# Kernel tuning notes

Measured on AMD Instinct MI355X. Metric: run time of the kernel, lower is better.

Reference implementation:

```python
import jax, jax.numpy as jnp
import numpy as np

B, S, D = 32, 256, 512   # batch, seq, shared_base hdim
N, H, O = 16, 256, 2     # num_tasks heads, adapter hidden, output_dim
VOCAB = 1024             # property-token lookup table length


def setup_inputs() -> dict:
    key = jax.random.key(0)
    ks = jax.random.split(key, 10)
    adapter_input = jax.random.normal(ks[0], (B, S, D), dtype=jnp.float32)
    tasks = jax.random.randint(ks[1], (B, S), 0, VOCAB, dtype=jnp.int64)
    lookup_table = jax.random.randint(ks[2], (VOCAB,), 0, N, dtype=jnp.int64)
    s1 = 1.0 / np.sqrt(D)
    s2 = 1.0 / np.sqrt(H)
    W1 = jax.random.uniform(ks[3], (N, D, H), jnp.float32, -s1, s1)
    b1 = jax.random.uniform(ks[4], (N, H), jnp.float32, -s1, s1)
    W2 = jax.random.uniform(ks[5], (N, H, H), jnp.float32, -s2, s2)
    b2 = jax.random.uniform(ks[6], (N, H), jnp.float32, -s2, s2)
    W3 = jax.random.uniform(ks[7], (N, H, O), jnp.float32, -s2, s2)
    b3 = jax.random.uniform(ks[8], (N, O), jnp.float32, -s2, s2)
    return dict(adapter_input=adapter_input, tasks=tasks, lookup_table=lookup_table,
                W1=W1, b1=b1, W2=W2, b2=b2, W3=W3, b3=b3)


def reference(adapter_input, tasks, lookup_table, W1, b1, W2, b2, W3, b3):
    # --- PropertyToIndexRouter: task token -> head index (-1 if out of range / unmapped)
    L = lookup_table.shape[0]
    clamped = jnp.clip(tasks, 0, L - 1)
    head_indices = lookup_table[clamped]
    invalid = (tasks >= L) | (tasks < 0)
    head_indices = jnp.where(invalid, -1, head_indices)          # [B, S]

    valid = head_indices >= 0
    idx = jnp.where(valid, head_indices, 0)                      # safe gather index

    # --- each head's SimpleAdapter run densely over all tokens (dropout=eval no-op),
    # vectorized over the head dim instead of a Python loop per head
    h1 = jax.nn.relu(jnp.einsum('bsd,ndh->bsnh', adapter_input, W1) + b1)   # [B,S,N,H]
    h2 = jax.nn.relu(jnp.einsum('bsnh,nhk->bsnk', h1, W2) + b2)             # [B,S,N,H]
    out_all = jnp.einsum('bsnk,nko->bsno', h2, W3) + b3                     # [B,S,N,O]

    # --- masked scatter-combine: pick each token's assigned head, zeros elsewhere
    out = jnp.take_along_axis(out_all, idx[:, :, None, None], axis=2)[:, :, 0, :]  # [B,S,O]
    out = jnp.where(valid[:, :, None], out, jnp.zeros((), out.dtype))
    return out
```

## Files before the change

### kernel.cpp

```cpp
#include <hip/hip_runtime.h>

#define TOK_TOTAL 8192
#define DDIM 512
#define HDIM 256
#define ODIM 2
#define NHEADS 16
#define VOCAB 1024

typedef __attribute__((ext_vector_type(8))) short short8;
typedef __attribute__((ext_vector_type(4))) float f32x4;
typedef __attribute__((ext_vector_type(4))) unsigned short ushort4v;

__device__ inline ushort f2bf(float f) {
    uint u = __float_as_uint(f);
    uint r = (u + 0x7fffu + ((u >> 16) & 1u)) >> 16;
    return (ushort)r;
}
__device__ inline float bf2f(ushort h) { return __uint_as_float(((uint)h) << 16); }

__global__ __launch_bounds__(256) void mth_prep_route(
    const float* __restrict__ W1, const float* __restrict__ W2,
    const int* __restrict__ tasks, const int* __restrict__ lut,
    ushort* __restrict__ W1h, ushort* __restrict__ W2h,
    int* __restrict__ counts, int* __restrict__ lists,
    float* __restrict__ out)
{
    const int b = blockIdx.x, t = threadIdx.x;

    if (b < 384) {
        __shared__ float s[32][257];
        const float* src;
        ushort* dh;
        if (b < 256) {
            const int n = b >> 4, kc = b & 15;
            src = W1 + (size_t)(n * 16 + kc) * 8192;
            dh  = W1h + (size_t)(n * 16 + kc) * 8192;
        } else {
            const int b2 = b - 256, n = b2 >> 3, kc = b2 & 7;
            src = W2 + (size_t)(n * 8 + kc) * 8192;
            dh  = W2h + (size_t)(n * 8 + kc) * 8192;
        }
        #pragma unroll
        for (int i = 0; i < 8; ++i) {
            const int q = t + i * 256;
            const float4 f = ((const float4*)src)[q];
            const int k = q >> 6, c4 = (q & 63) * 4;
            s[k][c4] = f.x; s[k][c4 + 1] = f.y; s[k][c4 + 2] = f.z; s[k][c4 + 3] = f.w;
        }
        __syncthreads();
        #pragma unroll
        for (int i = 0; i < 4; ++i) {
            const int s8 = t + i * 256;
            const int lidx = s8 & 63;
            const int c = (s8 >> 6) * 16 + (lidx & 15);
            const int kw = (lidx >> 4) * 8;
            short8 hb;
            #pragma unroll
            for (int j = 0; j < 8; ++j) hb[j] = (short)f2bf(s[kw + j][c]);
            *(short8*)(dh + (size_t)s8 * 8) = hb;
        }
        return;
    }

    const int i = b - 384;
    __shared__ int hist[16];
    __shared__ int wcnt[4][16];
    if (t < 16) hist[t] = 0;
    __syncthreads();
    for (int q = t; q < i * 256; q += 256) {
        const int task = tasks[q];
        const int h = (task >= 0 && task < VOCAB) ? lut[task] : -1;
        if (h >= 0) atomicAdd(&hist[h], 1);
    }
    const int tok = i * 256 + t;
    const int task = tasks[tok];
    const int h = (task >= 0 && task < VOCAB) ? lut[task] : -1;
    if (h < 0) {
        out[(size_t)tok * 2]     = 0.f;
        out[(size_t)tok * 2 + 1] = 0.f;
    }
    const int w = t >> 6, l = t & 63;
    const unsigned long long lt = (1ULL << l) - 1ULL;
    int pre = 0;
    #pragma unroll
    for (int n = 0; n < NHEADS; ++n) {
        const unsigned long long m = __ballot(h == n);
        if (h == n) pre = (int)__popcll(m & lt);
        if (l == 0) wcnt[w][n] = (int)__popcll(m);
    }
    __syncthreads();
    if (h >= 0) {
        int off = hist[h];
        for (int w2 = 0; w2 < w; ++w2) off += wcnt[w2][h];
        lists[h * TOK_TOTAL + off + pre] = tok;
    }
    if (i == 31 && t < 16) {
        int tot = hist[t];
        #pragma unroll
        for (int w2 = 0; w2 < 4; ++w2) tot += wcnt[w2][t];
        counts[t] = tot;
    }
}

__global__ __launch_bounds__(256) void mth_mlp4(
    const float* __restrict__ X, const int* __restrict__ counts,
    const int* __restrict__ lists,
    const ushort* __restrict__ W1h, const ushort* __restrict__ W2h,
    const float* __restrict__ b1, const float* __restrict__ b2,
    const float* __restrict__ W3, const float* __restrict__ b3,
    float* __restrict__ out)
{
    __shared__ __align__(16) ushort Ah[16][64][8];
    __shared__ __align__(16) ushort Al[16][64][8];
    __shared__ __align__(16) ushort Hh[8][64][8];
    __shared__ __align__(16) ushort Hl[8][64][8];
    __shared__ float part[4][16][2];

    const int b = blockIdx.x;
    const int n = ((b & 7) << 1) | ((b >> 3) & 1);
    const int tile0 = b >> 4;

    const int tid = threadIdx.x;
    const int w   = tid >> 6;
    const int l   = tid & 63;
    const int r16 = l & 15;
    const int kg  = l >> 4;

    const int cnt = counts[n];
    const int listbase = n * TOK_TOTAL;

    float bias1[4], bias2[4];
    float2 w3v[4];
    #pragma unroll
    for (int cf = 0; cf < 4; ++cf) {
        const int col = w * 64 + cf * 16 + r16;
        bias1[cf] = b1[n * HDIM + col];
        bias2[cf] = b2[n * HDIM + col];
        w3v[cf]   = *(const float2*)(W3 + (size_t)(n * HDIM + col) * 2);
    }
    const ushort* w1hn = W1h + (size_t)n * (16 * 8192);
    const ushort* w2hn = W2h + (size_t)n * (8 * 8192);
    const int le8 = l * 8;

    for (int T = tile0; T * 16 < cnt; T += 64) {
        #pragma unroll
        for (int p = 0; p < 8; ++p) {
            const int q   = tid + p * 256;
            const int row = q >> 7;
            const int f4  = q & 127;
            const int tokidx = min(T * 16 + row, cnt - 1);
            const int tok = lists[listbase + tokidx];
            const float4 f = *(const float4*)(X + (size_t)tok * DDIM + f4 * 4);
            const int kc  = f4 >> 3;
            const int kgw = (f4 >> 1) & 3;
            const int j0  = (f4 & 1) * 4;
            const int ln2 = (kgw * 16 + row) ^ (kc & 7);
            ushort4v hv, lv;
            const float vv[4] = {f.x, f.y, f.z, f.w};
            #pragma unroll
            for (int e = 0; e < 4; ++e) {
                const uint u = __float_as_uint(vv[e]);
                hv[e] = (ushort)(u >> 16);
                lv[e] = f2bf(vv[e] - __uint_as_float(u & 0xffff0000u));
            }
            *(ushort4v*)&Ah[kc][ln2][j0] = hv;
            *(ushort4v*)&Al[kc][ln2][j0] = lv;
        }
        __syncthreads();

        f32x4 acc[4];
        #pragma unroll
        for (int cf = 0; cf < 4; ++cf) acc[cf] = (f32x4){0.f, 0.f, 0.f, 0.f};

        #pragma unroll 4
        for (int kc = 0; kc < 16; ++kc) {
            const int ls = l ^ (kc & 7);
            const short8 ah = *(const short8*)&Ah[kc][ls][0];
            const short8 al = *(const short8*)&Al[kc][ls][0];
            const ushort* bp = w1hn + kc * 8192 + le8;
            #pragma unroll
            for (int cf = 0; cf < 4; ++cf) {
                const short8 bh = *(const short8*)(bp + (w * 4 + cf) * 512);
                acc[cf] = __builtin_amdgcn_mfma_f32_16x16x32_bf16(ah, bh, acc[cf], 0, 0, 0);
                acc[cf] = __builtin_amdgcn_mfma_f32_16x16x32_bf16(al, bh, acc[cf], 0, 0, 0);
            }
        }

        #pragma unroll
        for (int cf = 0; cf < 4; ++cf) {
            const int kc2 = 2 * w + (cf >> 1);
            const int lp  = ((cf & 1) * 2 + (r16 >> 3)) * 16;
            const int e   = r16 & 7;
            #pragma unroll
            for (int j = 0; j < 4; ++j) {
                const float v = fmaxf(acc[cf][j] + bias1[cf], 0.f);
                const uint u = __float_as_uint(v);
                Hh[kc2][lp + kg * 4 + j][e] = (ushort)(u >> 16);
                Hl[kc2][lp + kg * 4 + j][e] =
                    f2bf(v - __uint_as_float(u & 0xffff0000u));
            }
        }
        __syncthreads();

        f32x4 acc2[4];
        #pragma unroll
        for (int cf = 0; cf < 4; ++cf) acc2[cf] = (f32x4){0.f, 0.f, 0.f, 0.f};

        #pragma unroll 4
        for (int kc = 0; kc < 8; ++kc) {
            const short8 ah = *(const short8*)&Hh[kc][l][0];
            const short8 al = *(const short8*)&Hl[kc][l][0];
            const ushort* bp = w2hn + kc * 8192 + le8;
            #pragma unroll
            for (int cf = 0; cf < 4; ++cf) {
                const short8 bh = *(const short8*)(bp + (w * 4 + cf) * 512);
                acc2[cf] = __builtin_amdgcn_mfma_f32_16x16x32_bf16(ah, bh, acc2[cf], 0, 0, 0);
                acc2[cf] = __builtin_amdgcn_mfma_f32_16x16x32_bf16(al, bh, acc2[cf], 0, 0, 0);
            }
        }

        float p[4][2];
        #pragma unroll
        for (int j = 0; j < 4; ++j) { p[j][0] = 0.f; p[j][1] = 0.f; }
        #pragma unroll
        for (int cf = 0; cf < 4; ++cf) {
            #pragma unroll
            for (int j = 0; j < 4; ++j) {
                const float v = fmaxf(acc2[cf][j] + bias2[cf], 0.f);
                p[j][0] = fmaf(v, w3v[cf].x, p[j][0]);
                p[j][1] = fmaf(v, w3v[cf].y, p[j][1]);
            }
        }
        #pragma unroll
        for (int off = 8; off >= 1; off >>= 1) {
            #pragma unroll
            for (int j = 0; j < 4; ++j) {
                p[j][0] += __shfl_xor(p[j][0], off);
                p[j][1] += __shfl_xor(p[j][1], off);
            }
        }
        if (r16 == 0) {
            #pragma unroll
            for (int j = 0; j < 4; ++j) {
                part[w][kg * 4 + j][0] = p[j][0];
                part[w][kg * 4 + j][1] = p[j][1];
            }
        }
        __syncthreads();

        if (tid < 32) {
            const int tk = tid >> 1, o = tid & 1;
            if (T * 16 + tk < cnt) {
                const float s = part[0][tk][o] + part[1][tk][o] +
                                part[2][tk][o] + part[3][tk][o];
                const int tok = lists[listbase + T * 16 + tk];
                out[(size_t)tok * 2 + o] = s + b3[n * 2 + o];
            }
        }
        __syncthreads();
    }
}

#define CHUNKS 16
#define CHUNK (TOK_TOTAL / CHUNKS)
#define TILE 32
#define KB 16

__global__ __launch_bounds__(256) void mth_routed_fp32(
    const float* __restrict__ X, const int* __restrict__ tasks,
    const int* __restrict__ lut,
    const float* __restrict__ W1, const float* __restrict__ b1,
    const float* __restrict__ W2, const float* __restrict__ b2,
    const float* __restrict__ W3, const float* __restrict__ b3,
    float* __restrict__ out)
{
    const int n = blockIdx.x, chnk = blockIdx.y, tid = threadIdx.x;
    const int lane = tid & 63, wv = tid >> 6, tx = tid & 31, ty = tid >> 5;
    __shared__ int s_list[CHUNK];
    __shared__ int s_cnt[8];
    __shared__ __align__(16) float s_x[KB][TILE];
    __shared__ __align__(16) float s_w[KB][HDIM];
    __shared__ __align__(16) float s_h[HDIM][TILE];
    const int base = chnk * CHUNK;
    int mytok[2], mypre[2], myseg[2]; bool mymatch[2];
    #pragma unroll
    for (int i = 0; i < 2; ++i) {
        const int tok = base + i * 256 + tid;
        const int task = tasks[tok];
        const int hidx = (task >= 0 && task < VOCAB) ? lut[task] : -1;
        const bool match = (hidx == n);
        const unsigned long long mask = __ballot(match);
        mytok[i] = tok; mymatch[i] = match;
        mypre[i] = __popcll(mask & ((1ULL << lane) - 1ULL));
        myseg[i] = i * 4 + wv;
        if (lane == 0) s_cnt[i * 4 + wv] = (int)__popcll(mask);
    }
    __syncthreads();
    int total = 0; int myoff[2] = {0, 0};
    #pragma unroll
    for (int s2 = 0; s2 < 8; ++s2) {
        if (s2 == myseg[0]) myoff[0] = total;
        if (s2 == myseg[1]) myoff[1] = total;
        total += s_cnt[s2];
    }
    #pragma unroll
    for (int i = 0; i < 2; ++i)
        if (mymatch[i]) s_list[myoff[i] + mypre[i]] = mytok[i];
    __syncthreads();
    const int ntok = total;
    if (ntok == 0) return;
    float bias1[8], bias2[8];
    #pragma unroll
    for (int j = 0; j < 8; ++j) {
        bias1[j] = b1[n * HDIM + tx * 8 + j];
        bias2[j] = b2[n * HDIM + tx * 8 + j];
    }
    float w3v[16];
    #pragma unroll
    for (int j = 0; j < 16; ++j) w3v[j] = W3[n * HDIM * ODIM + tx * 8 * ODIM + j];
    const float b3v0 = b3[n * ODIM + 0], b3v1 = b3[n * ODIM + 1];
    const float* W1n = W1 + (size_t)n * DDIM * HDIM;
    const float* W2n = W2 + (size_t)n * HDIM * HDIM;
    for (int ts = 0; ts < ntok; ts += TILE) {
        const int m = min(TILE, ntok - ts);
        float acc[4][8];
        #pragma unroll
        for (int t = 0; t < 4; ++t)
            #pragma unroll
            for (int j = 0; j < 8; ++j) acc[t][j] = 0.f;
        for (int kc = 0; kc < DDIM / KB; ++kc) {
            const float4* src = (const float4*)(W1n + kc * KB * HDIM);
            float4* dst = (float4*)s_w;
            #pragma unroll
            for (int p = 0; p < 4; ++p) dst[tid + p * 256] = src[tid + p * 256];
            #pragma unroll
            for (int p = 0; p < 2; ++p) {
                const int e = tid + p * 256;
                const int dd = e >> 5, t = e & 31;
                float v = 0.f;
                if (t < m) v = X[(size_t)s_list[ts + t] * DDIM + kc * KB + dd];
                s_x[dd][t] = v;
            }
            __syncthreads();
            #pragma unroll
            for (int dd = 0; dd < KB; ++dd) {
                const float4 xa = *(const float4*)&s_x[dd][ty * 4];
                const float4 wa = *(const float4*)&s_w[dd][tx * 8];
                const float4 wb = *(const float4*)&s_w[dd][tx * 8 + 4];
                const float xs[4] = {xa.x, xa.y, xa.z, xa.w};
                const float ws[8] = {wa.x, wa.y, wa.z, wa.w, wb.x, wb.y, wb.z, wb.w};
                #pragma unroll
                for (int t = 0; t < 4; ++t)
                    #pragma unroll
                    for (int j = 0; j < 8; ++j) acc[t][j] = fmaf(xs[t], ws[j], acc[t][j]);
            }
            __syncthreads();
        }
        #pragma unroll
        for (int j = 0; j < 8; ++j) {
            float4 v;
            v.x = fmaxf(acc[0][j] + bias1[j], 0.f);
            v.y = fmaxf(acc[1][j] + bias1[j], 0.f);
            v.z = fmaxf(acc[2][j] + bias1[j], 0.f);
            v.w = fmaxf(acc[3][j] + bias1[j], 0.f);
            *(float4*)&s_h[tx * 8 + j][ty * 4] = v;
        }
        __syncthreads();
        float acc2[4][8];
        #pragma unroll
        for (int t = 0; t < 4; ++t)
            #pragma unroll
            for (int j = 0; j < 8; ++j) acc2[t][j] = 0.f;
        for (int kc = 0; kc < HDIM / KB; ++kc) {
            const float4* src = (const float4*)(W2n + kc * KB * HDIM);
            float4* dst = (float4*)s_w;
            #pragma unroll
            for (int p = 0; p < 4; ++p) dst[tid + p * 256] = src[tid + p * 256];
            __syncthreads();
            #pragma unroll
            for (int dd = 0; dd < KB; ++dd) {
                const int k = kc * KB + dd;
                const float4 xa = *(const float4*)&s_h[k][ty * 4];
                const float4 wa = *(const float4*)&s_w[dd][tx * 8];
                const float4 wb = *(const float4*)&s_w[dd][tx * 8 + 4];
                const float xs[4] = {xa.x, xa.y, xa.z, xa.w};
                const float ws[8] = {wa.x, wa.y, wa.z, wa.w, wb.x, wb.y, wb.z, wb.w};
                #pragma unroll
                for (int t = 0; t < 4; ++t)
                    #pragma unroll
                    for (int j = 0; j < 8; ++j) acc2[t][j] = fmaf(xs[t], ws[j], acc2[t][j]);
            }
            __syncthreads();
        }
        float p0[4] = {0.f, 0.f, 0.f, 0.f}, p1[4] = {0.f, 0.f, 0.f, 0.f};
        #pragma unroll
        for (int t = 0; t < 4; ++t)
            #pragma unroll
            for (int j = 0; j < 8; ++j) {
                const float v = fmaxf(acc2[t][j] + bias2[j], 0.f);
                p0[t] = fmaf(v, w3v[j * 2 + 0], p0[t]);
                p1[t] = fmaf(v, w3v[j * 2 + 1], p1[t]);
            }
        #pragma unroll
        for (int off = 16; off > 0; off >>= 1)
            #pragma unroll
            for (int t = 0; t < 4; ++t) {
                p0[t] += __shfl_xor(p0[t], off);
                p1[t] += __shfl_xor(p1[t], off);
            }
        if (tx == 0) {
            #pragma unroll
            for (int t = 0; t < 4; ++t) {
                const int ti = ty * 4 + t;
                if (ti < m) {
                    const int tok = s_list[ts + ti];
                    out[tok * ODIM + 0] = p0[t] + b3v0;
                    out[tok * ODIM + 1] = p1[t] + b3v1;
                }
            }
        }
        __syncthreads();
    }
}

extern "C" void kernel_launch(void* const* d_in, const int* in_sizes, int n_in,
                              void* d_out, int out_size, void* d_ws, size_t ws_size,
                              hipStream_t stream) {
    (void)in_sizes; (void)n_in;
    const float* X     = (const float*)d_in[0];
    const int*   tasks = (const int*)d_in[1];
    const int*   lut   = (const int*)d_in[2];
    const float* W1    = (const float*)d_in[3];
    const float* b1    = (const float*)d_in[4];
    const float* W2    = (const float*)d_in[5];
    const float* b2    = (const float*)d_in[6];
    const float* W3    = (const float*)d_in[7];
    const float* b3    = (const float*)d_in[8];
    float* out = (float*)d_out;

    const size_t OFF_COUNTS = 0;
    const size_t OFF_LISTS  = 64;
    const size_t OFF_W1H    = OFF_LISTS + (size_t)NHEADS * TOK_TOTAL * 4;
    const size_t NW1        = (size_t)NHEADS * DDIM * HDIM;
    const size_t NW2        = (size_t)NHEADS * HDIM * HDIM;
    const size_t OFF_W2H    = OFF_W1H + NW1 * 2;
    const size_t NEED       = OFF_W2H + NW2 * 2;

    if (ws_size < NEED) {
        hipMemsetAsync(out, 0, (size_t)out_size * sizeof(float), stream);
        dim3 grid(NHEADS, CHUNKS);
        mth_routed_fp32<<<grid, 256, 0, stream>>>(X, tasks, lut, W1, b1, W2, b2, W3, b3, out);
        return;
    }

    char* ws = (char*)d_ws;
    int*    counts = (int*)(ws + OFF_COUNTS);
    int*    lists  = (int*)(ws + OFF_LISTS);
    ushort* W1h    = (ushort*)(ws + OFF_W1H);
    ushort* W2h    = (ushort*)(ws + OFF_W2H);

    mth_prep_route<<<416, 256, 0, stream>>>(W1, W2, tasks, lut,
                                            W1h, W2h, counts, lists, out);
    mth_mlp4<<<1024, 256, 0, stream>>>(X, counts, lists, W1h, W2h,
                                       b1, b2, W3, b3, out);
}
```

Before: 33.98 us.

## Process 32-token tiles per block with 8 waves sharing weight loads

The MLP kernel now uses 512-thread blocks that handle two 16-token sub-tiles at once. Waves are split into a token half and a column group, so each block's W1/W2 fragment loads serve twice as many tokens. The grid shrinks from 1024 to 256 blocks. This roughly halves per-token global weight traffic and the per-tile sync and epilogue overhead, but gives fewer blocks, doubles LDS per block, and wastes more padding work for heads with small token counts.

After: 41.94 us. +23.4%, slower.

```diff
diff --git a/kernel.cpp b/kernel.cpp
--- a/kernel.cpp
+++ b/kernel.cpp
@@ -102,7 +102,7 @@
     }
 }
 
-__global__ __launch_bounds__(256) void mth_mlp4(
+__global__ __launch_bounds__(512) void mth_mlp5(
     const float* __restrict__ X, const int* __restrict__ counts,
     const int* __restrict__ lists,
     const ushort* __restrict__ W1h, const ushort* __restrict__ W2h,
@@ -110,11 +110,11 @@
     const float* __restrict__ W3, const float* __restrict__ b3,
     float* __restrict__ out)
 {
-    __shared__ __align__(16) ushort Ah[16][64][8];
-    __shared__ __align__(16) ushort Al[16][64][8];
-    __shared__ __align__(16) ushort Hh[8][64][8];
-    __shared__ __align__(16) ushort Hl[8][64][8];
-    __shared__ float part[4][16][2];
+    __shared__ __align__(16) ushort Ah[16][2][64][8];
+    __shared__ __align__(16) ushort Al[16][2][64][8];
+    __shared__ __align__(16) ushort Hh[8][2][64][8];
+    __shared__ __align__(16) ushort Hl[8][2][64][8];
+    __shared__ float part[8][16][2];
 
     const int b = blockIdx.x;
     const int n = ((b & 7) << 1) | ((b >> 3) & 1);
@@ -122,6 +122,8 @@
 
     const int tid = threadIdx.x;
     const int w   = tid >> 6;
+    const int tf  = w >> 2;
+    const int cg  = w & 3;
     const int l   = tid & 63;
     const int r16 = l & 15;
     const int kg  = l >> 4;
@@ -133,7 +135,7 @@
     float2 w3v[4];
     #pragma unroll
     for (int cf = 0; cf < 4; ++cf) {
-        const int col = w * 64 + cf * 16 + r16;
+        const int col = cg * 64 + cf * 16 + r16;
         bias1[cf] = b1[n * HDIM + col];
         bias2[cf] = b2[n * HDIM + col];
         w3v[cf]   = *(const float2*)(W3 + (size_t)(n * HDIM + col) * 2);
@@ -142,19 +144,21 @@
     const ushort* w2hn = W2h + (size_t)n * (8 * 8192);
     const int le8 = l * 8;
 
-    for (int T = tile0; T * 16 < cnt; T += 64) {
+    for (int T = tile0; T * 32 < cnt; T += 16) {
         #pragma unroll
         for (int p = 0; p < 8; ++p) {
-            const int q   = tid + p * 256;
+            const int q   = tid + p * 512;
             const int row = q >> 7;
             const int f4  = q & 127;
-            const int tokidx = min(T * 16 + row, cnt - 1);
+            const int tokidx = min(T * 32 + row, cnt - 1);
             const int tok = lists[listbase + tokidx];
             const float4 f = *(const float4*)(X + (size_t)tok * DDIM + f4 * 4);
             const int kc  = f4 >> 3;
             const int kgw = (f4 >> 1) & 3;
             const int j0  = (f4 & 1) * 4;
-            const int ln2 = (kgw * 16 + row) ^ (kc & 7);
+            const int tfs = row >> 4;
+            const int rs  = row & 15;
+            const int ln2 = (kgw * 16 + rs) ^ (kc & 7);
             ushort4v hv, lv;
             const float vv[4] = {f.x, f.y, f.z, f.w};
             #pragma unroll
@@ -163,8 +167,8 @@
                 hv[e] = (ushort)(u >> 16);
                 lv[e] = f2bf(vv[e] - __uint_as_float(u & 0xffff0000u));
             }
-            *(ushort4v*)&Ah[kc][ln2][j0] = hv;
-            *(ushort4v*)&Al[kc][ln2][j0] = lv;
+            *(ushort4v*)&Ah[kc][tfs][ln2][j0] = hv;
+            *(ushort4v*)&Al[kc][tfs][ln2][j0] = lv;
         }
         __syncthreads();
 
@@ -175,12 +179,12 @@
         #pragma unroll 4
         for (int kc = 0; kc < 16; ++kc) {
             const int ls = l ^ (kc & 7);
-            const short8 ah = *(const short8*)&Ah[kc][ls][0];
-            const short8 al = *(const short8*)&Al[kc][ls][0];
+            const short8 ah = *(const short8*)&Ah[kc][tf][ls][0];
+            const short8 al = *(const short8*)&Al[kc][tf][ls][0];
             const ushort* bp = w1hn + kc * 8192 + le8;
             #pragma unroll
             for (int cf = 0; cf < 4; ++cf) {
-                const short8 bh = *(const short8*)(bp + (w * 4 + cf) * 512);
+                const short8 bh = *(const short8*)(bp + (cg * 4 + cf) * 512);
                 acc[cf] = __builtin_amdgcn_mfma_f32_16x16x32_bf16(ah, bh, acc[cf], 0, 0, 0);
                 acc[cf] = __builtin_amdgcn_mfma_f32_16x16x32_bf16(al, bh, acc[cf], 0, 0, 0);
             }
@@ -188,15 +192,15 @@
 
         #pragma unroll
         for (int cf = 0; cf < 4; ++cf) {
-            const int kc2 = 2 * w + (cf >> 1);
+            const int kc2 = 2 * cg + (cf >> 1);
             const int lp  = ((cf & 1) * 2 + (r16 >> 3)) * 16;
             const int e   = r16 & 7;
             #pragma unroll
             for (int j = 0; j < 4; ++j) {
                 const float v = fmaxf(acc[cf][j] + bias1[cf], 0.f);
                 const uint u = __float_as_uint(v);
-                Hh[kc2][lp + kg * 4 + j][e] = (ushort)(u >> 16);
-                Hl[kc2][lp + kg * 4 + j][e] =
+                Hh[kc2][tf][lp + kg * 4 + j][e] = (ushort)(u >> 16);
+                Hl[kc2][tf][lp + kg * 4 + j][e] =
                     f2bf(v - __uint_as_float(u & 0xffff0000u));
             }
         }
@@ -208,12 +212,12 @@
 
         #pragma unroll 4
         for (int kc = 0; kc < 8; ++kc) {
-            const short8 ah = *(const short8*)&Hh[kc][l][0];
-            const short8 al = *(const short8*)&Hl[kc][l][0];
+            const short8 ah = *(const short8*)&Hh[kc][tf][l][0];
+            const short8 al = *(const short8*)&Hl[kc][tf][l][0];
             const ushort* bp = w2hn + kc * 8192 + le8;
             #pragma unroll
             for (int cf = 0; cf < 4; ++cf) {
-                const short8 bh = *(const short8*)(bp + (w * 4 + cf) * 512);
+                const short8 bh = *(const short8*)(bp + (cg * 4 + cf) * 512);
                 acc2[cf] = __builtin_amdgcn_mfma_f32_16x16x32_bf16(ah, bh, acc2[cf], 0, 0, 0);
                 acc2[cf] = __builtin_amdgcn_mfma_f32_16x16x32_bf16(al, bh, acc2[cf], 0, 0, 0);
             }
@@ -248,12 +252,13 @@
         }
         __syncthreads();
 
-        if (tid < 32) {
+        if (tid < 64) {
             const int tk = tid >> 1, o = tid & 1;
-            if (T * 16 + tk < cnt) {
-                const float s = part[0][tk][o] + part[1][tk][o] +
-                                part[2][tk][o] + part[3][tk][o];
-                const int tok = lists[listbase + T * 16 + tk];
+            if (T * 32 + tk < cnt) {
+                const int tfh = tk >> 4, r = tk & 15;
+                const float s = part[tfh * 4 + 0][r][o] + part[tfh * 4 + 1][r][o] +
+                                part[tfh * 4 + 2][r][o] + part[tfh * 4 + 3][r][o];
+                const int tok = lists[listbase + T * 32 + tk];
                 out[(size_t)tok * 2 + o] = s + b3[n * 2 + o];
             }
         }
@@ -461,6 +466,6 @@
 
     mth_prep_route<<<416, 256, 0, stream>>>(W1, W2, tasks, lut,
                                             W1h, W2h, counts, lists, out);
-    mth_mlp4<<<1024, 256, 0, stream>>>(X, counts, lists, W1h, W2h,
-                                       b1, b2, W3, b3, out);
+    mth_mlp5<<<256, 512, 0, stream>>>(X, counts, lists, W1h, W2h,
+                                      b1, b2, W3, b3, out);
 }
```
